# Kernel optimization log

Hardware: AMD Instinct MI355X
Metric: run time of the kernel (lower is better)

Reference implementation:

```python
import jax, jax.numpy as jnp
import numpy as np
import math

NUM_HEADS = 16
D_MODEL = 1024
LN_EPS = 1e-5


def _layer_norm(x, g, b):
    mu = jnp.mean(x, axis=-1, keepdims=True)
    var = jnp.mean((x - mu) ** 2, axis=-1, keepdims=True)
    return (x - mu) / jnp.sqrt(var + LN_EPS) * g + b


def setup_inputs() -> dict:
    key = jax.random.key(0)
    ks = jax.random.split(key, 12)
    B, H, W, d = 32, 16, 16, D_MODEL
    P, F = 64, 128
    s = 0.02
    return {
        "x": jax.random.normal(ks[0], (B, H, W, d), jnp.float32),
        "pattern_features": jax.random.normal(ks[1], (B, P, F), jnp.float32),
        "wq": jax.random.normal(ks[2], (d, d), jnp.float32) * s,
        "bq": jnp.zeros((d,), jnp.float32),
        "wk": jax.random.normal(ks[3], (d, d), jnp.float32) * s,
        "bk": jnp.zeros((d,), jnp.float32),
        "wv": jax.random.normal(ks[4], (d, d), jnp.float32) * s,
        "bv": jnp.zeros((d,), jnp.float32),
        "wo": jax.random.normal(ks[5], (d, d), jnp.float32) * s,
        "bo": jnp.zeros((d,), jnp.float32),
        "ln_g": jnp.ones((d,), jnp.float32),
        "ln_b": jnp.zeros((d,), jnp.float32),
    }


def reference(x, pattern_features, wq, bq, wk, bk, wv, bv, wo, bo, ln_g, ln_b):
    B, H, W, d = x.shape
    S = H * W
    nh = NUM_HEADS
    dk = d // nh
    x_seq = x.reshape(B, S, d)

    def proj(w, b):
        return (x_seq @ w.T + b).reshape(B, S, nh, dk).transpose(0, 2, 1, 3)  # (B,nh,S,dk)

    q, k, v = proj(wq, bq), proj(wk, bk), proj(wv, bv)
    scores = jnp.einsum("bhsd,bhtd->bhst", q, k) / math.sqrt(dk)  # (B,nh,S,S)

    # creative bias: diversity bonus on top-left min(S,64) block, same for all heads
    m = min(S, 64)
    sim = jnp.einsum("bpf,bqf->bpq", pattern_features, pattern_features)
    div = 1.0 - jax.nn.softmax(sim, axis=-1)  # (B,P,P)
    bias = jnp.zeros((B, nh, S, S), x.dtype)
    bias = bias.at[:, :, :m, :m].set(div[:, None, :m, :m] * 0.1)

    # faithful to torch: scores + bias.unsqueeze(0) -> rank-5 (1,B,nh,S,S)
    scores5 = scores[None] + bias[None]
    aw = jax.nn.softmax(scores5, axis=-1)
    attn = jnp.matmul(aw, v)  # (1,B,nh,S,dk) via broadcasting
    # faithful to torch transpose(1,2).view(B,S,d): row-major reshape of (1,nh,B,S,dk)
    attn = jnp.transpose(attn, (0, 2, 1, 3, 4)).reshape(B, S, d)

    out = attn @ wo.T + bo
    out = _layer_norm(out + x_seq, ln_g, ln_b)

    attention_weights = jax.nn.softmax(scores, axis=-1).mean(axis=1)  # (B,S,S)
    return out.reshape(B, H, W, d), attention_weights
```

## Files before the change

### kernel.cpp

```cpp
#include <hip/hip_runtime.h>

typedef unsigned short u16;
typedef unsigned int   u32;
typedef short bf16x8 __attribute__((ext_vector_type(8)));
typedef float f32x4  __attribute__((ext_vector_type(4)));

__device__ __forceinline__ float bf2f(u16 u){
  union { u32 u; float f; } c; c.u = ((u32)u) << 16; return c.f;
}
__device__ __forceinline__ u16 f2bf(float f){
  union { float f; u32 u; } c; c.f = f;
  u32 u = c.u + 0x7fffu + ((c.u >> 16) & 1u);
  return (u16)(u >> 16);
}

__device__ __forceinline__ void gload16(const u16* g, u16* l){
  __builtin_amdgcn_global_load_lds((const __attribute__((address_space(1))) u32*)g,
                                   (__attribute__((address_space(3))) u32*)l, 16, 0, 0);
}

__device__ __forceinline__ float waveRed(float v, int ismax){
  #pragma unroll
  for (int o = 32; o > 0; o >>= 1){
    float t = __shfl_xor(v, o, 64);
    v = ismax ? fmaxf(v, t) : (v + t);
  }
  return v;
}
__device__ __forceinline__ float blockRed(float v, int ismax, float* red, int tid){
  v = waveRed(v, ismax);
  __syncthreads();
  if ((tid & 63) == 0) red[tid >> 6] = v;
  __syncthreads();
  return ismax ? fmaxf(fmaxf(red[0], red[1]), fmaxf(red[2], red[3]))
               : (red[0] + red[1] + red[2] + red[3]);
}

__global__ __launch_bounds__(256)
void conv_all(const float* __restrict__ x, const float* __restrict__ w0,
              const float* __restrict__ w1, const float* __restrict__ w2,
              const float* __restrict__ w3, u16* __restrict__ xdst,
              u16* __restrict__ wdst){
  const int bid = blockIdx.x;
  const float* s;
  u16* d;
  size_t i;
  if (bid < 4096){
    s = x; d = xdst;
    i = ((size_t)bid * 256 + threadIdx.x) * 8;
  } else {
    const int wb = bid - 4096;
    const int wi = wb >> 9;
    s = wi == 0 ? w0 : (wi == 1 ? w1 : (wi == 2 ? w2 : w3));
    d = wdst + (size_t)wi * 1048576;
    i = ((size_t)(wb & 511) * 256 + threadIdx.x) * 8;
  }
  const float4 a = *(const float4*)(s + i);
  const float4 b = *(const float4*)(s + i + 4);
  uint4 o;
  o.x = (u32)f2bf(a.x) | ((u32)f2bf(a.y) << 16);
  o.y = (u32)f2bf(a.z) | ((u32)f2bf(a.w) << 16);
  o.z = (u32)f2bf(b.x) | ((u32)f2bf(b.y) << 16);
  o.w = (u32)f2bf(b.z) | ((u32)f2bf(b.w) << 16);
  *(uint4*)(d + i) = o;
}

__global__ __launch_bounds__(256)
void div_kernel(const float* __restrict__ pf, float* __restrict__ divp)
{
  __shared__ float pfs[64][129];
  __shared__ float svs[64][65];
  const int b = blockIdx.x;
  const int tid = threadIdx.x;
  const float* pb = pf + (size_t)b * 8192;
  for (int i = tid; i < 8192; i += 256) pfs[i >> 7][i & 127] = pb[i];
  __syncthreads();
  const int p = tid & 63, qg = tid >> 6;
  for (int qq = qg * 16; qq < qg * 16 + 16; ++qq){
    float a = 0.f;
    #pragma unroll 8
    for (int f = 0; f < 128; ++f) a += pfs[p][f] * pfs[qq][f];
    svs[p][qq] = a;
  }
  __syncthreads();
  if (tid < 64){
    float m = -1e30f;
    for (int qq = 0; qq < 64; ++qq) m = fmaxf(m, svs[tid][qq]);
    float s = 0.f;
    for (int qq = 0; qq < 64; ++qq){ const float e = __expf(svs[tid][qq] - m); svs[tid][qq] = e; s += e; }
    const float inv = 1.f / s;
    float* dr = divp + ((size_t)b * 64 + tid) * 64;
    for (int qq = 0; qq < 64; ++qq) dr[qq] = 0.1f * (1.f - svs[tid][qq] * inv);
  }
}

template<int MODE>
__global__ __launch_bounds__(256, 3)
void gemm_lds(const u16* __restrict__ A, const u16* __restrict__ Wb,
              const float* __restrict__ bias0, const float* __restrict__ bias1,
              const float* __restrict__ bias2, void* __restrict__ outp)
{
  __shared__ u16 As[3][4096];
  __shared__ u16 Bs[3][4096];
  const int tid = threadIdx.x, lane = tid & 63, w = tid >> 6;
  const int wm = (w >> 1) * 64, wn = (w & 1) * 64;
  const int bm = blockIdx.x;
  int bn = blockIdx.y;
  const u16* Wp = Wb;
  const float* bias = bias0;
  float scale = 1.f;
  int wsel = 0;
  if (MODE == 0){
    wsel = bn >> 3; bn &= 7;
    Wp = Wb + (size_t)wsel * 1048576;
    bias = wsel == 0 ? bias0 : (wsel == 1 ? bias1 : bias2);
    if (wsel == 0) scale = 0.125f;
  }
  const bool vsw = (MODE == 0 && wsel == 2);
  const int mt  = vsw ? bn : bm;
  const int nt2 = vsw ? bm : bn;
  const u16* MA = vsw ? Wp : A;
  const u16* MB = vsw ? A  : Wp;

  const f32x4 z = {0.f, 0.f, 0.f, 0.f};
  f32x4 acc[4][4];
  #pragma unroll
  for (int i = 0; i < 4; ++i)
    #pragma unroll
    for (int j = 0; j < 4; ++j) acc[i][j] = z;

  const int r4  = lane >> 2;
  const int c8s = (((lane & 3) ^ ((lane >> 3) & 3)) * 8);
  const int ca0 = w * 2, ca1 = w * 2 + 1;
  const u16* gA0 = MA + (size_t)(mt  * 128 + ca0 * 16 + r4) * 1024 + c8s;
  const u16* gA1 = MA + (size_t)(mt  * 128 + ca1 * 16 + r4) * 1024 + c8s;
  const u16* gB0 = MB + (size_t)(nt2 * 128 + ca0 * 16 + r4) * 1024 + c8s;
  const u16* gB1 = MB + (size_t)(nt2 * 128 + ca1 * 16 + r4) * 1024 + c8s;
  const int lo0 = ca0 * 512 + lane * 8;
  const int lo1 = ca1 * 512 + lane * 8;

  const int fr = lane & 15, quad = lane >> 4;
  int offA[4], offB[4];
  #pragma unroll
  for (int i = 0; i < 4; ++i){
    const int r = wm + i * 16 + fr;
    offA[i] = r * 32 + ((quad ^ ((r >> 1) & 3)) * 8);
  }
  #pragma unroll
  for (int j = 0; j < 4; ++j){
    const int r = wn + j * 16 + fr;
    offB[j] = r * 32 + ((quad ^ ((r >> 1) & 3)) * 8);
  }

#define STG(s, kk) \
    gload16(gA0 + (kk), &As[s][lo0]); \
    gload16(gA1 + (kk), &As[s][lo1]); \
    gload16(gB0 + (kk), &Bs[s][lo0]); \
    gload16(gB1 + (kk), &Bs[s][lo1]);

  STG(0, 0)
  STG(1, 32)
  asm volatile("s_waitcnt vmcnt(4)" ::: "memory");
  __builtin_amdgcn_sched_barrier(0);
  __builtin_amdgcn_s_barrier();
  asm volatile("" ::: "memory");
  __builtin_amdgcn_sched_barrier(0);

  int slot = 0;
  #pragma unroll 1
  for (int t = 0; t < 32; ++t){
    const int s2 = slot < 1 ? 2 : slot - 1;
    if (t < 30){ STG(s2, (t + 2) * 32) }
    const u16* as_ = As[slot];
    const u16* bs_ = Bs[slot];
    bf16x8 af[4], bfv[4];
    #pragma unroll
    for (int i = 0; i < 4; ++i) af[i]  = *(const bf16x8*)&as_[offA[i]];
    #pragma unroll
    for (int j = 0; j < 4; ++j) bfv[j] = *(const bf16x8*)&bs_[offB[j]];
    __builtin_amdgcn_s_setprio(1);
    #pragma unroll
    for (int i = 0; i < 4; ++i)
      #pragma unroll
      for (int j = 0; j < 4; ++j)
        acc[i][j] = __builtin_amdgcn_mfma_f32_16x16x32_bf16(af[i], bfv[j], acc[i][j], 0, 0, 0);
    __builtin_amdgcn_s_setprio(0);
    if (t < 30)       { asm volatile("s_waitcnt vmcnt(4)" ::: "memory"); }
    else if (t == 30) { asm volatile("s_waitcnt vmcnt(0)" ::: "memory"); }
    if (t < 31){
      __builtin_amdgcn_sched_barrier(0);
      __builtin_amdgcn_s_barrier();
      asm volatile("" ::: "memory");
      __builtin_amdgcn_sched_barrier(0);
    }
    slot = slot == 2 ? 0 : slot + 1;
  }
#undef STG

  #pragma unroll
  for (int i = 0; i < 4; ++i){
    #pragma unroll
    for (int j = 0; j < 4; ++j){
      const int gr0 = mt  * 128 + wm + i * 16 + quad * 4;
      const int gc  = nt2 * 128 + wn + j * 16 + fr;
      if (vsw){
        const int bb = gc >> 8, s = gc & 255;
        #pragma unroll
        for (int r = 0; r < 4; ++r){
          const int grow = gr0 + r;
          const int h = grow >> 6, kk = grow & 63;
          ((u16*)outp)[(size_t)2 * 8388608 + (size_t)bb * 262144 +
                       (size_t)h * 16384 + (size_t)kk * 256 + s] =
            f2bf(acc[i][j][r] + bias[grow]);
        }
      } else {
        const float bvv = bias[gc];
        #pragma unroll
        for (int r = 0; r < 4; ++r){
          const int gr = gr0 + r;
          const float val = (acc[i][j][r] + bvv) * scale;
          if (MODE == 0){
            const int b = gr >> 8, s = gr & 255, h = gc >> 6, kk = gc & 63;
            ((u16*)outp)[(size_t)wsel * 8388608 + (size_t)b * 262144 +
                         (size_t)h * 16384 + (size_t)s * 64 + kk] = f2bf(val);
          } else {
            ((float*)outp)[(size_t)gr * 1024 + gc] = val;
          }
        }
      }
    }
  }
}

__global__ __launch_bounds__(256, 2)
void attn_aw(const u16* __restrict__ q, const u16* __restrict__ k,
             const u16* __restrict__ vT, const float* __restrict__ divp,
             u16* __restrict__ attn_s, float* __restrict__ aw)
{
  __shared__ __align__(16) u16 Ps[4][16][136];
  const int raw = blockIdx.x;
  const int blk = (raw & 7) * 64 + (raw >> 3);
  const int b = blk >> 4, st = blk & 15;
  const int tid = threadIdx.x, lane = tid & 63, w = tid >> 6;
  const int quad = lane >> 4, l15 = lane & 15;
  const int rowb = st * 16;
  const f32x4 z = {0.f, 0.f, 0.f, 0.f};
  float awacc[16][4] = {};

  #pragma unroll 1
  for (int hi = 0; hi < 4; ++hi){
    const int h = hi * 4 + w;
    const u16* qh = q  + ((size_t)b * 16 + h) * 16384;
    const u16* kh = k  + ((size_t)b * 16 + h) * 16384;
    const u16* vh = vT + ((size_t)b * 16 + h) * 16384;
    const bf16x8 af0 = *(const bf16x8*)(qh + (size_t)(rowb + l15) * 64 + quad * 8);
    const bf16x8 af1 = *(const bf16x8*)(qh + (size_t)(rowb + l15) * 64 + 32 + quad * 8);
    f32x4 sc[16];
    #pragma unroll
    for (int ct = 0; ct < 16; ++ct){
      const bf16x8 b0 = *(const bf16x8*)(kh + (size_t)(ct * 16 + l15) * 64 + quad * 8);
      const bf16x8 b1 = *(const bf16x8*)(kh + (size_t)(ct * 16 + l15) * 64 + 32 + quad * 8);
      f32x4 a = __builtin_amdgcn_mfma_f32_16x16x32_bf16(af0, b0, z, 0, 0, 0);
      sc[ct]  = __builtin_amdgcn_mfma_f32_16x16x32_bf16(af1, b1, a, 0, 0, 0);
    }
    float rs[4];
    if (st < 4){
      #pragma unroll
      for (int rr = 0; rr < 4; ++rr){
        float m = sc[0][rr];
        #pragma unroll
        for (int ct = 1; ct < 16; ++ct) m = fmaxf(m, sc[ct][rr]);
        #pragma unroll
        for (int o = 1; o < 16; o <<= 1) m = fmaxf(m, __shfl_xor(m, o, 64));
        float s = 0.f;
        #pragma unroll
        for (int ct = 0; ct < 16; ++ct) s += __expf(sc[ct][rr] - m);
        #pragma unroll
        for (int o = 1; o < 16; o <<= 1) s += __shfl_xor(s, o, 64);
        const float inv = 1.f / s;
        #pragma unroll
        for (int ct = 0; ct < 16; ++ct)
          awacc[ct][rr] += __expf(sc[ct][rr] - m) * inv;
      }
      const float* dv = divp + (size_t)b * 4096 + (size_t)(rowb + quad * 4) * 64 + l15;
      #pragma unroll
      for (int ct = 0; ct < 4; ++ct)
        #pragma unroll
        for (int rr = 0; rr < 4; ++rr)
          sc[ct][rr] += dv[rr * 64 + ct * 16];
      #pragma unroll
      for (int rr = 0; rr < 4; ++rr){
        float m = sc[0][rr];
        #pragma unroll
        for (int ct = 1; ct < 16; ++ct) m = fmaxf(m, sc[ct][rr]);
        #pragma unroll
        for (int o = 1; o < 16; o <<= 1) m = fmaxf(m, __shfl_xor(m, o, 64));
        float s = 0.f;
        #pragma unroll
        for (int ct = 0; ct < 16; ++ct){
          const float e = __expf(sc[ct][rr] - m); sc[ct][rr] = e; s += e;
        }
        #pragma unroll
        for (int o = 1; o < 16; o <<= 1) s += __shfl_xor(s, o, 64);
        rs[rr] = 1.f / s;
      }
    } else {
      #pragma unroll
      for (int rr = 0; rr < 4; ++rr){
        float m = sc[0][rr];
        #pragma unroll
        for (int ct = 1; ct < 16; ++ct) m = fmaxf(m, sc[ct][rr]);
        #pragma unroll
        for (int o = 1; o < 16; o <<= 1) m = fmaxf(m, __shfl_xor(m, o, 64));
        float s = 0.f;
        #pragma unroll
        for (int ct = 0; ct < 16; ++ct){
          const float e = __expf(sc[ct][rr] - m); sc[ct][rr] = e; s += e;
        }
        #pragma unroll
        for (int o = 1; o < 16; o <<= 1) s += __shfl_xor(s, o, 64);
        rs[rr] = 1.f / s;
        #pragma unroll
        for (int ct = 0; ct < 16; ++ct)
          awacc[ct][rr] += sc[ct][rr] * rs[rr];
      }
    }
    f32x4 o4[4] = {z, z, z, z};
    #pragma unroll
    for (int half = 0; half < 2; ++half){
      #pragma unroll
      for (int ct = 0; ct < 8; ++ct)
        #pragma unroll
        for (int rr = 0; rr < 4; ++rr)
          Ps[w][quad * 4 + rr][ct * 16 + l15] = f2bf(sc[half * 8 + ct][rr] * rs[rr]);
      #pragma unroll
      for (int kc = 0; kc < 4; ++kc){
        const bf16x8 pa = *(const bf16x8*)&Ps[w][l15][kc * 32 + quad * 8];
        #pragma unroll
        for (int nt = 0; nt < 4; ++nt){
          const bf16x8 vb8 = *(const bf16x8*)(vh + (size_t)(nt * 16 + l15) * 256 +
                                              half * 128 + kc * 32 + quad * 8);
          o4[nt] = __builtin_amdgcn_mfma_f32_16x16x32_bf16(pa, vb8, o4[nt], 0, 0, 0);
        }
      }
    }
    const size_t rbase = ((size_t)(512 * h + 16 * b + st)) * 1024;
    #pragma unroll
    for (int nt = 0; nt < 4; ++nt)
      #pragma unroll
      for (int rr = 0; rr < 4; ++rr)
        attn_s[rbase + (size_t)(quad * 4 + rr) * 64 + nt * 16 + l15] = f2bf(o4[nt][rr]);
  }

  float* awl = (float*)&Ps[0][0][0];
  const size_t base = (size_t)b * 65536 + (size_t)rowb * 256;
  #pragma unroll
  for (int cc = 0; cc < 4; ++cc){
    __syncthreads();
    #pragma unroll
    for (int j = 0; j < 4; ++j)
      #pragma unroll
      for (int rr = 0; rr < 4; ++rr)
        awl[(w * 16 + quad * 4 + rr) * 68 + j * 16 + l15] = awacc[cc * 4 + j][rr];
    __syncthreads();
    const int idx = tid * 4;
    const int row = idx >> 6, col = idx & 63;
    const float4 a0 = *(const float4*)&awl[(      row) * 68 + col];
    const float4 a1 = *(const float4*)&awl[(16  + row) * 68 + col];
    const float4 a2 = *(const float4*)&awl[(32  + row) * 68 + col];
    const float4 a3 = *(const float4*)&awl[(48  + row) * 68 + col];
    float4 o;
    o.x = (a0.x + a1.x + a2.x + a3.x) * 0.0625f;
    o.y = (a0.y + a1.y + a2.y + a3.y) * 0.0625f;
    o.z = (a0.z + a1.z + a2.z + a3.z) * 0.0625f;
    o.w = (a0.w + a1.w + a2.w + a3.w) * 0.0625f;
    *(float4*)(aw + base + (size_t)row * 256 + cc * 64 + col) = o;
  }
}

__global__ __launch_bounds__(256)
void ln_kernel(const float* __restrict__ y2, const float* __restrict__ x,
               const float* __restrict__ g, const float* __restrict__ bb,
               float* __restrict__ outp)
{
  __shared__ float red[4];
  const int r = blockIdx.x, tid = threadIdx.x;
  const float4 yv = ((const float4*)(y2 + (size_t)r * 1024))[tid];
  const float4 xv = ((const float4*)(x  + (size_t)r * 1024))[tid];
  const float v0 = yv.x + xv.x;
  const float v1 = yv.y + xv.y;
  const float v2 = yv.z + xv.z;
  const float v3 = yv.w + xv.w;
  const float ssum = blockRed(v0 + v1 + v2 + v3, 0, red, tid);
  const float mu = ssum * (1.f / 1024.f);
  const float d0 = v0 - mu, d1 = v1 - mu, d2 = v2 - mu, d3 = v3 - mu;
  const float sq = blockRed(d0 * d0 + d1 * d1 + d2 * d2 + d3 * d3, 0, red, tid);
  const float rstd = rsqrtf(sq * (1.f / 1024.f) + 1e-5f);
  const float4 gv = ((const float4*)g)[tid];
  const float4 bv = ((const float4*)bb)[tid];
  float4 o;
  o.x = d0 * rstd * gv.x + bv.x;
  o.y = d1 * rstd * gv.y + bv.y;
  o.z = d2 * rstd * gv.z + bv.z;
  o.w = d3 * rstd * gv.w + bv.w;
  ((float4*)(outp + (size_t)r * 1024))[tid] = o;
}

extern "C" void kernel_launch(void* const* d_in, const int* in_sizes, int n_in,
                              void* d_out, int out_size, void* d_ws, size_t ws_size,
                              hipStream_t stream)
{
  int ix = -1, ipf = -1, iw[4] = {-1,-1,-1,-1}, iv[6] = {-1,-1,-1,-1,-1,-1};
  int nw = 0, nv = 0;
  for (int i = 0; i < n_in; ++i){
    const int sz = in_sizes[i];
    if (sz == 8388608 && ix < 0) ix = i;
    else if (sz == 262144 && ipf < 0) ipf = i;
    else if (sz == 1048576 && nw < 4) iw[nw++] = i;
    else if (sz == 1024 && nv < 6) iv[nv++] = i;
  }
  if (ix < 0 || ipf < 0 || nw != 4 || nv != 6){
    ix = 0; ipf = 1; iw[0] = 2; iv[0] = 3; iw[1] = 4; iv[1] = 5;
    iw[2] = 6; iv[2] = 7; iw[3] = 8; iv[3] = 9; iv[4] = 10; iv[5] = 11;
  }

  const float* x   = (const float*)d_in[ix];
  const float* pf  = (const float*)d_in[ipf];
  const float* wq  = (const float*)d_in[iw[0]];
  const float* wk  = (const float*)d_in[iw[1]];
  const float* wv  = (const float*)d_in[iw[2]];
  const float* wo  = (const float*)d_in[iw[3]];
  const float* bq  = (const float*)d_in[iv[0]];
  const float* bk  = (const float*)d_in[iv[1]];
  const float* bv  = (const float*)d_in[iv[2]];
  const float* bo  = (const float*)d_in[iv[3]];
  const float* lng = (const float*)d_in[iv[4]];
  const float* lnb = (const float*)d_in[iv[5]];

  float* out0   = (float*)d_out;
  float* aw_out = out0 + 8388608;

  u16* x_bf = (u16*)d_out;
  u16* attn = x_bf + 8388608;
  u16* qkv    = (u16*)d_ws;
  float* divp = (float*)((char*)d_ws + (size_t)48 * 1048576);
  u16* warena = (u16*)((char*)d_ws + (size_t)49 * 1048576);
  float* y2   = (float*)d_ws;

  conv_all<<<6144, 256, 0, stream>>>(x, wq, wk, wv, wo, x_bf, warena);
  div_kernel<<<32, 256, 0, stream>>>(pf, divp);

  gemm_lds<0><<<dim3(64, 24), 256, 0, stream>>>(x_bf, warena, bq, bk, bv, (void*)qkv);

  u16* qw = qkv, *kw = qkv + 8388608, *vw = qkv + 16777216;
  attn_aw<<<512, 256, 0, stream>>>(qw, kw, vw, divp, attn, aw_out);

  gemm_lds<1><<<dim3(64, 8), 256, 0, stream>>>(attn, warena + 3145728, bo, nullptr, nullptr, (void*)y2);
  ln_kernel<<<8192, 256, 0, stream>>>(y2, x, lng, lnb, out0);
}
```

Baseline: 325.3 us.

## Split attention heads across two blocks and combine averaged weights in a separate kernel

Each attention block now handles 8 heads instead of 16, which doubles the grid from 512 to 1024 blocks to fill the GPU's compute units better. Each half writes an unnormalised partial head-sum of the attention weights into scratch space in the output buffer, reusing memory that held the bf16 copy of x. A new combine kernel adds the two partials and applies the 1/16 mean. This costs extra global traffic for the partials and one more kernel launch.

```diff
diff --git a/kernel.cpp b/kernel.cpp
--- a/kernel.cpp
+++ b/kernel.cpp
@@ -235,12 +235,13 @@
 __global__ __launch_bounds__(256, 2)
 void attn_aw(const u16* __restrict__ q, const u16* __restrict__ k,
              const u16* __restrict__ vT, const float* __restrict__ divp,
-             u16* __restrict__ attn_s, float* __restrict__ aw)
+             u16* __restrict__ attn_s, float* __restrict__ aw_part)
 {
   __shared__ __align__(16) u16 Ps[4][16][136];
   const int raw = blockIdx.x;
-  const int blk = (raw & 7) * 64 + (raw >> 3);
-  const int b = blk >> 4, st = blk & 15;
+  const int blk = (raw & 7) * 128 + (raw >> 3);
+  const int hp = blk & 1, bst = blk >> 1;
+  const int b = bst >> 4, st = bst & 15;
   const int tid = threadIdx.x, lane = tid & 63, w = tid >> 6;
   const int quad = lane >> 4, l15 = lane & 15;
   const int rowb = st * 16;
@@ -248,8 +249,8 @@
   float awacc[16][4] = {};
 
   #pragma unroll 1
-  for (int hi = 0; hi < 4; ++hi){
-    const int h = hi * 4 + w;
+  for (int hi = 0; hi < 2; ++hi){
+    const int h = hp * 8 + hi * 4 + w;
     const u16* qh = q  + ((size_t)b * 16 + h) * 16384;
     const u16* kh = k  + ((size_t)b * 16 + h) * 16384;
     const u16* vh = vT + ((size_t)b * 16 + h) * 16384;
@@ -353,6 +354,7 @@
   }
 
   float* awl = (float*)&Ps[0][0][0];
+  float* awp = aw_part + (size_t)hp * 2097152;
   const size_t base = (size_t)b * 65536 + (size_t)rowb * 256;
   #pragma unroll
   for (int cc = 0; cc < 4; ++cc){
@@ -370,12 +372,26 @@
     const float4 a2 = *(const float4*)&awl[(32  + row) * 68 + col];
     const float4 a3 = *(const float4*)&awl[(48  + row) * 68 + col];
     float4 o;
-    o.x = (a0.x + a1.x + a2.x + a3.x) * 0.0625f;
-    o.y = (a0.y + a1.y + a2.y + a3.y) * 0.0625f;
-    o.z = (a0.z + a1.z + a2.z + a3.z) * 0.0625f;
-    o.w = (a0.w + a1.w + a2.w + a3.w) * 0.0625f;
-    *(float4*)(aw + base + (size_t)row * 256 + cc * 64 + col) = o;
-  }
+    o.x = a0.x + a1.x + a2.x + a3.x;
+    o.y = a0.y + a1.y + a2.y + a3.y;
+    o.z = a0.z + a1.z + a2.z + a3.z;
+    o.w = a0.w + a1.w + a2.w + a3.w;
+    *(float4*)(awp + base + (size_t)row * 256 + cc * 64 + col) = o;
+  }
+}
+
+__global__ __launch_bounds__(256)
+void combine_aw(const float* __restrict__ p, float* __restrict__ aw)
+{
+  const size_t i = ((size_t)blockIdx.x * 256 + threadIdx.x) * 4;
+  const float4 a = *(const float4*)(p + i);
+  const float4 b = *(const float4*)(p + 2097152 + i);
+  float4 o;
+  o.x = (a.x + b.x) * 0.0625f;
+  o.y = (a.y + b.y) * 0.0625f;
+  o.z = (a.z + b.z) * 0.0625f;
+  o.w = (a.w + b.w) * 0.0625f;
+  *(float4*)(aw + i) = o;
 }
 
 __global__ __launch_bounds__(256)
@@ -442,6 +458,7 @@
 
   u16* x_bf = (u16*)d_out;
   u16* attn = x_bf + 8388608;
+  float* aw_p = (float*)d_out;
   u16* qkv    = (u16*)d_ws;
   float* divp = (float*)((char*)d_ws + (size_t)48 * 1048576);
   u16* warena = (u16*)((char*)d_ws + (size_t)49 * 1048576);
@@ -453,7 +470,8 @@
   gemm_lds<0><<<dim3(64, 24), 256, 0, stream>>>(x_bf, warena, bq, bk, bv, (void*)qkv);
 
   u16* qw = qkv, *kw = qkv + 8388608, *vw = qkv + 16777216;
-  attn_aw<<<512, 256, 0, stream>>>(qw, kw, vw, divp, attn, aw_out);
+  attn_aw<<<1024, 256, 0, stream>>>(qw, kw, vw, divp, attn, aw_p);
+  combine_aw<<<2048, 256, 0, stream>>>(aw_p, aw_out);
 
   gemm_lds<1><<<dim3(64, 8), 256, 0, stream>>>(attn, warena + 3145728, bo, nullptr, nullptr, (void*)y2);
   ln_kernel<<<8192, 256, 0, stream>>>(y2, x, lng, lnb, out0);
```

New measurement: 340.3 us. 1.05x slower.
